# Kernel optimization log

Hardware: AMD Instinct MI355X
Metric: run time of the kernel (lower is better)

## Reference

```python
import jax, jax.numpy as jnp
import numpy as np


def setup_inputs() -> dict:
    key = jax.random.key(0)
    k1, k2, k3, k4 = jax.random.split(key, 4)
    B, C_ORIG, H, W = 64, 448, 56, 56
    C = 100
    P = H * W
    feats = jax.random.normal(k1, (B, C_ORIG, H, W), dtype=jnp.float32)
    mean = jax.random.normal(k2, (P, C), dtype=jnp.float32)
    icov = jax.random.normal(k3, (P, C, C), dtype=jnp.float32)
    sel_idx = jnp.sort(jax.random.randint(k4, (C,), 0, C_ORIG, dtype=jnp.int64))
    return {"feats": feats, "mean": mean, "icov": icov, "sel_idx": sel_idx,
            "image_size": 224}


def reference(feats, mean, icov, sel_idx, image_size):
    # feats: [B, C_orig, H, W]; select the PaDiM random channel subset -> [B, C, H, W]
    f = feats[:, sel_idx]
    B, C, H, W = f.shape
    # [B, H*W, C] patch-major layout as in the torch code
    f = jnp.transpose(f, (0, 2, 3, 1)).reshape(B, H * W, C)
    # Per-patch Mahalanobis distance, fully batched over all H*W patches
    # (replaces the Python loop of H*W small einsums in the original).
    diff = f - mean[None]                                   # [B, P, C]
    dist = jnp.einsum('bpi,pij,bpj->bp', diff, icov, diff)  # [B, P]
    score_map = dist.reshape(B, H, W)
    # Bilinear upsample to input resolution (align_corners=False ~ half-pixel)
    score_map = jax.image.resize(score_map, (B, image_size, image_size),
                                 method='bilinear')
    return score_map
```

## Files before the change

kernel.cpp:

```cpp
#include <hip/hip_runtime.h>
#include <hip/hip_bf16.h>

#define B_N     64
#define C_ORIG  448
#define C_SEL   100
#define CPD     112
#define HW      3136
#define IMG     224

typedef short bf16x8 __attribute__((ext_vector_type(8)));
typedef float f32x4  __attribute__((ext_vector_type(4)));

static __device__ __forceinline__ unsigned pkbf(float x, float y) {
    union { __hip_bfloat162 h; unsigned u; } c;
    c.h = __float22bfloat162_rn(float2{x, y});
    return c.u;
}
static __device__ __forceinline__ float bf2f(unsigned short h) {
    return __uint_as_float(((unsigned int)h) << 16);
}

__global__ __launch_bounds__(256) void kA_gather(const float* __restrict__ feats,
                                                 const float* __restrict__ mean,
                                                 const int* __restrict__ sel,
                                                 unsigned short* __restrict__ D)
{
    __shared__ unsigned short Dt[64 * 128];
    char* DtB = reinterpret_cast<char*>(Dt);
    const int tid = threadIdx.x;
    const int p0  = blockIdx.x * 64;
    const int b   = blockIdx.y;

    if (tid < 192) {
        int pr = tid / 3, un = 25 + tid % 3;
        *reinterpret_cast<uint2*>(DtB + pr * 256 + ((8 * un) ^ ((pr & 31) << 3)))
            = make_uint2(0u, 0u);
    }

    const int w    = tid >> 6;
    const int lane = tid & 63;
    const float* fb   = feats + (size_t)b * (C_ORIG * HW) + p0 + lane;
    const float* mrow = mean + (size_t)(p0 + lane) * C_SEL;
    const unsigned swz = (unsigned)(lane & 31) << 3;
    char* rowB = DtB + lane * 256;

    auto quad = [&](int c0) {
        int ch0 = sel[c0], ch1 = sel[c0 + 1], ch2 = sel[c0 + 2], ch3 = sel[c0 + 3];
        float4 m4 = *reinterpret_cast<const float4*>(mrow + c0);
        float v0 = fb[(size_t)ch0 * HW] - m4.x;
        float v1 = fb[(size_t)ch1 * HW] - m4.y;
        float v2 = fb[(size_t)ch2 * HW] - m4.z;
        float v3 = fb[(size_t)ch3 * HW] - m4.w;
        uint2 pk = make_uint2(pkbf(v0, v1), pkbf(v2, v3));
        *reinterpret_cast<uint2*>(rowB + (((unsigned)(2 * c0)) ^ swz)) = pk;
    };

    if (w < 3) {
#pragma unroll
        for (int q = 0; q < 6; ++q) quad(w * 24 + q * 4);
    } else {
#pragma unroll
        for (int q = 0; q < 7; ++q) quad(72 + q * 4);
    }
    __syncthreads();

    unsigned short* Dp = D + ((size_t)p0 * B_N + b) * CPD;
#pragma unroll
    for (int q = 0; q < 4; ++q) {
        int unit = tid + q * 256;
        if (unit < 896) {
            int pr = unit / 14;
            int s  = unit % 14;
            unsigned off = ((unsigned)(16 * s)) ^ ((((unsigned)pr & 31u) << 3) & 0xF0u);
            uint4 v = *reinterpret_cast<const uint4*>(DtB + pr * 256 + off);
            uint4 r = (pr & 1) ? make_uint4(v.z, v.w, v.x, v.y) : v;
            *reinterpret_cast<uint4*>(reinterpret_cast<char*>(Dp)
                + (size_t)pr * (B_N * CPD * 2) + s * 16) = r;
        }
    }
}

__global__ __launch_bounds__(256, 5) void kB_maha(const float* __restrict__ icov,
                                                  const unsigned short* __restrict__ D,
                                                  float* __restrict__ dist)
{
    __shared__ unsigned short Mb[112 * 128];
    char* MbB = reinterpret_cast<char*>(Mb);
    const int tid  = threadIdx.x;
    const int p    = blockIdx.x;
    const int w    = tid >> 6;
    const int lane = tid & 63;
    const int lrow = lane & 15;
    const int g    = lane >> 4;
    const int bcol = w * 16 + lrow;
    const unsigned short* Drow = D + ((size_t)p * B_N + bcol) * CPD;

    bf16x8 bfr[4];
#pragma unroll
    for (int ks = 0; ks < 4; ++ks)
        bfr[ks] = *reinterpret_cast<const bf16x8*>(Drow + ks * 32 + g * 8);
    ushort4 dvec[7];
#pragma unroll
    for (int it = 0; it < 7; ++it)
        dvec[it] = *reinterpret_cast<const ushort4*>(Drow + it * 16 + g * 4);

#pragma unroll
    for (int q = 0; q < 3; ++q) {
        int z = tid + q * 256;
        if (z < 700) {
            int i = z / 7, un = 25 + z % 7;
            *reinterpret_cast<uint2*>(MbB + i * 256 + ((8 * un) ^ ((i & 7) << 4)))
                = make_uint2(0u, 0u);
        }
    }
#pragma unroll
    for (int q = 0; q < 2; ++q) {
        int z = tid + q * 256;
        if (z < 384) {
            int i = 100 + (z >> 5), un = z & 31;
            *reinterpret_cast<uint2*>(MbB + i * 256 + ((8 * un) ^ ((i & 7) << 4)))
                = make_uint2(0u, 0u);
        }
    }
    const float4* src = reinterpret_cast<const float4*>(icov + (size_t)p * (C_SEL * C_SEL));
#pragma unroll
    for (int q = 0; q < 10; ++q) {
        int idx4 = tid + q * 256;
        if (idx4 < 2500) {
            float4 v = src[idx4];
            int i = idx4 / 25, un = idx4 % 25;
            uint2 pk = make_uint2(pkbf(v.x, v.y), pkbf(v.z, v.w));
            *reinterpret_cast<uint2*>(MbB + i * 256 + ((8 * un) ^ ((i & 7) << 4))) = pk;
        }
    }
    __syncthreads();

    f32x4 acc[7];
#pragma unroll
    for (int it = 0; it < 7; ++it) acc[it] = (f32x4){0.f, 0.f, 0.f, 0.f};

#pragma unroll
    for (int ks = 0; ks < 4; ++ks) {
#pragma unroll
        for (int it = 0; it < 7; ++it) {
            int i = it * 16 + lrow;
            bf16x8 afrag = *reinterpret_cast<const bf16x8*>(
                MbB + i * 256 + ((ks * 64 + g * 16) ^ ((i & 7) << 4)));
            acc[it] = __builtin_amdgcn_mfma_f32_16x16x32_bf16(afrag, bfr[ks], acc[it], 0, 0, 0);
        }
    }

    float partial = 0.f;
#pragma unroll
    for (int it = 0; it < 7; ++it) {
#pragma unroll
        for (int r = 0; r < 4; ++r) {
            int i = it * 16 + g * 4 + r;
            if (i < C_SEL) {
                unsigned short dh = (r == 0) ? dvec[it].x : (r == 1) ? dvec[it].y
                                   : (r == 2) ? dvec[it].z : dvec[it].w;
                partial += acc[it][r] * bf2f(dh);
            }
        }
    }
    partial += __shfl_xor(partial, 16);
    partial += __shfl_xor(partial, 32);
    if (g == 0) dist[(size_t)bcol * HW + p] = partial;
}

__global__ __launch_bounds__(256) void kC_resize(const float* __restrict__ dist,
                                                 float* __restrict__ out)
{
    int gid = blockIdx.x * 256 + threadIdx.x;
    int m = gid % 56;
    int t = gid / 56;
    int y = t % IMG;
    int b = t / IMG;

    float sy = y * 0.25f - 0.375f;
    float fy0 = floorf(sy);
    float fy = sy - fy0;
    int y0 = max((int)fy0, 0);
    int y1 = min((int)fy0 + 1, 55);
    int xm1 = max(m - 1, 0);
    int xp1 = min(m + 1, 55);

    const float* db = dist + (size_t)b * HW;
    const float* d0 = db + y0 * 56;
    const float* d1 = db + y1 * 56;
    float a0 = d0[xm1], b0 = d0[m], c0 = d0[xp1];
    float a1 = d1[xm1], b1 = d1[m], c1 = d1[xp1];

    float A  = a0 + fy * (a1 - a0);
    float Bv = b0 + fy * (b1 - b0);
    float Cv = c0 + fy * (c1 - c0);

    float4 o;
    o.x = A  + 0.625f * (Bv - A);
    o.y = A  + 0.875f * (Bv - A);
    o.z = Bv + 0.125f * (Cv - Bv);
    o.w = Bv + 0.375f * (Cv - Bv);
    *reinterpret_cast<float4*>(out + ((size_t)b * IMG + y) * IMG + 4 * m) = o;
}

extern "C" void kernel_launch(void* const* d_in, const int* in_sizes, int n_in,
                              void* d_out, int out_size, void* d_ws, size_t ws_size,
                              hipStream_t stream)
{
    const float* feats = (const float*)d_in[0];
    const float* mean  = (const float*)d_in[1];
    const float* icov  = (const float*)d_in[2];
    const int*   sel   = (const int*)d_in[3];
    float* out = (float*)d_out;

    unsigned short* Dws = (unsigned short*)d_ws;
    float* distws = (float*)((char*)d_ws + (size_t)HW * B_N * CPD * 2);

    dim3 gA(49, B_N);
    kA_gather<<<gA, 256, 0, stream>>>(feats, mean, sel, Dws);
    kB_maha<<<HW, 256, 0, stream>>>(icov, Dws, distws);
    kC_resize<<<3136, 256, 0, stream>>>(distws, out);
}
```

Baseline: 78.42 us.

## Transpose mean, store dist patch-major, and tile resize through LDS

A new pre-kernel transposes mean to channel-major so the gather kernel reads it coalesced across lanes, where it previously used strided float4 row loads. The Mahalanobis kernel now writes dist as [P][B] so its per-patch stores are contiguous, and the dvec loads move after the LDS fill. The resize kernel now runs one block per output row, staging two source rows for all batches in padded shared memory before interpolating. The cost is an extra launch and workspace buffer, and the resize grid shrinks to 224 blocks, which lowers parallelism.

```diff
diff --git a/kernel.cpp b/kernel.cpp
--- a/kernel.cpp
+++ b/kernel.cpp
@@ -20,8 +20,39 @@
     return __uint_as_float(((unsigned int)h) << 16);
 }
 
+__global__ __launch_bounds__(256) void kA0_meanT(const float* __restrict__ mean,
+                                                 float* __restrict__ meanT)
+{
+    __shared__ float mt[64 * 100];
+    const int tid = threadIdx.x;
+    const int p0  = blockIdx.x * 64;
+    const float4* src = reinterpret_cast<const float4*>(mean + (size_t)p0 * C_SEL);
+#pragma unroll
+    for (int q = 0; q < 7; ++q) {
+        int idx4 = tid + q * 256;
+        if (idx4 < 1600) {
+            float4 v = src[idx4];
+            *reinterpret_cast<float4*>(&mt[idx4 * 4]) = v;
+        }
+    }
+    __syncthreads();
+#pragma unroll
+    for (int q = 0; q < 7; ++q) {
+        int u = tid + q * 256;
+        if (u < 1600) {
+            int c = u >> 4, s = u & 15;
+            float4 v;
+            v.x = mt[(s * 4 + 0) * 100 + c];
+            v.y = mt[(s * 4 + 1) * 100 + c];
+            v.z = mt[(s * 4 + 2) * 100 + c];
+            v.w = mt[(s * 4 + 3) * 100 + c];
+            *reinterpret_cast<float4*>(meanT + (size_t)c * HW + p0 + s * 4) = v;
+        }
+    }
+}
+
 __global__ __launch_bounds__(256) void kA_gather(const float* __restrict__ feats,
-                                                 const float* __restrict__ mean,
+                                                 const float* __restrict__ meanT,
                                                  const int* __restrict__ sel,
                                                  unsigned short* __restrict__ D)
 {
@@ -39,18 +70,17 @@
 
     const int w    = tid >> 6;
     const int lane = tid & 63;
-    const float* fb   = feats + (size_t)b * (C_ORIG * HW) + p0 + lane;
-    const float* mrow = mean + (size_t)(p0 + lane) * C_SEL;
+    const float* fb = feats + (size_t)b * (C_ORIG * HW) + p0 + lane;
+    const float* mb = meanT + p0 + lane;
     const unsigned swz = (unsigned)(lane & 31) << 3;
     char* rowB = DtB + lane * 256;
 
     auto quad = [&](int c0) {
         int ch0 = sel[c0], ch1 = sel[c0 + 1], ch2 = sel[c0 + 2], ch3 = sel[c0 + 3];
-        float4 m4 = *reinterpret_cast<const float4*>(mrow + c0);
-        float v0 = fb[(size_t)ch0 * HW] - m4.x;
-        float v1 = fb[(size_t)ch1 * HW] - m4.y;
-        float v2 = fb[(size_t)ch2 * HW] - m4.z;
-        float v3 = fb[(size_t)ch3 * HW] - m4.w;
+        float v0 = fb[(size_t)ch0 * HW] - mb[(size_t)(c0 + 0) * HW];
+        float v1 = fb[(size_t)ch1 * HW] - mb[(size_t)(c0 + 1) * HW];
+        float v2 = fb[(size_t)ch2 * HW] - mb[(size_t)(c0 + 2) * HW];
+        float v3 = fb[(size_t)ch3 * HW] - mb[(size_t)(c0 + 3) * HW];
         uint2 pk = make_uint2(pkbf(v0, v1), pkbf(v2, v3));
         *reinterpret_cast<uint2*>(rowB + (((unsigned)(2 * c0)) ^ swz)) = pk;
     };
@@ -99,10 +129,6 @@
 #pragma unroll
     for (int ks = 0; ks < 4; ++ks)
         bfr[ks] = *reinterpret_cast<const bf16x8*>(Drow + ks * 32 + g * 8);
-    ushort4 dvec[7];
-#pragma unroll
-    for (int it = 0; it < 7; ++it)
-        dvec[it] = *reinterpret_cast<const ushort4*>(Drow + it * 16 + g * 4);
 
 #pragma unroll
     for (int q = 0; q < 3; ++q) {
@@ -135,6 +161,11 @@
     }
     __syncthreads();
 
+    ushort4 dvec[7];
+#pragma unroll
+    for (int it = 0; it < 7; ++it)
+        dvec[it] = *reinterpret_cast<const ushort4*>(Drow + it * 16 + g * 4);
+
     f32x4 acc[7];
 #pragma unroll
     for (int it = 0; it < 7; ++it) acc[it] = (f32x4){0.f, 0.f, 0.f, 0.f};
@@ -165,42 +196,64 @@
     }
     partial += __shfl_xor(partial, 16);
     partial += __shfl_xor(partial, 32);
-    if (g == 0) dist[(size_t)bcol * HW + p] = partial;
+    if (g == 0) dist[p * B_N + bcol] = partial;
 }
 
 __global__ __launch_bounds__(256) void kC_resize(const float* __restrict__ dist,
                                                  float* __restrict__ out)
 {
-    int gid = blockIdx.x * 256 + threadIdx.x;
-    int m = gid % 56;
-    int t = gid / 56;
-    int y = t % IMG;
-    int b = t / IMG;
+    __shared__ float L[2 * 56 * 66];
+    const int tid = threadIdx.x;
+    const int y   = blockIdx.x;
 
     float sy = y * 0.25f - 0.375f;
     float fy0 = floorf(sy);
     float fy = sy - fy0;
     int y0 = max((int)fy0, 0);
     int y1 = min((int)fy0 + 1, 55);
-    int xm1 = max(m - 1, 0);
-    int xp1 = min(m + 1, 55);
-
-    const float* db = dist + (size_t)b * HW;
-    const float* d0 = db + y0 * 56;
-    const float* d1 = db + y1 * 56;
-    float a0 = d0[xm1], b0 = d0[m], c0 = d0[xp1];
-    float a1 = d1[xm1], b1 = d1[m], c1 = d1[xp1];
-
-    float A  = a0 + fy * (a1 - a0);
-    float Bv = b0 + fy * (b1 - b0);
-    float Cv = c0 + fy * (c1 - c0);
-
-    float4 o;
-    o.x = A  + 0.625f * (Bv - A);
-    o.y = A  + 0.875f * (Bv - A);
-    o.z = Bv + 0.125f * (Cv - Bv);
-    o.w = Bv + 0.375f * (Cv - Bv);
-    *reinterpret_cast<float4*>(out + ((size_t)b * IMG + y) * IMG + 4 * m) = o;
+    int rsrc[2] = {y0, y1};
+
+#pragma unroll
+    for (int r = 0; r < 2; ++r) {
+        const float4* s4 = reinterpret_cast<const float4*>(dist + (size_t)rsrc[r] * 56 * B_N);
+#pragma unroll
+        for (int j = 0; j < 4; ++j) {
+            int idx = tid + j * 256;
+            if (idx < 896) {
+                float4 v = s4[idx];
+                int m  = idx >> 4;
+                int b4 = (idx & 15) * 4;
+                float* d = &L[r * 56 * 66 + m * 66 + b4];
+                d[0] = v.x; d[1] = v.y; d[2] = v.z; d[3] = v.w;
+            }
+        }
+    }
+    __syncthreads();
+
+#pragma unroll
+    for (int j = 0; j < 14; ++j) {
+        int unit = tid + j * 256;
+        int b = unit / 56;
+        int m = unit % 56;
+        int xm1 = max(m - 1, 0);
+        int xp1 = min(m + 1, 55);
+
+        const float* L0 = &L[0 * 56 * 66];
+        const float* L1 = &L[1 * 56 * 66];
+        float a0 = L0[xm1 * 66 + b], b0 = L0[m * 66 + b], c0 = L0[xp1 * 66 + b];
+        float a1 = L1[xm1 * 66 + b], b1 = L1[m * 66 + b], c1 = L1[xp1 * 66 + b];
+
+        float A  = a0 + fy * (a1 - a0);
+        float Bv = b0 + fy * (b1 - b0);
+        float Cv = c0 + fy * (c1 - c0);
+
+        float4 o;
+        o.x = A  + 0.625f * (Bv - A);
+        o.y = A  + 0.875f * (Bv - A);
+        o.z = Bv + 0.125f * (Cv - Bv);
+        o.w = Bv + 0.375f * (Cv - Bv);
+        *reinterpret_cast<float4*>(out + ((size_t)b * IMG + y) * IMG + 4 * m) = o;
+    }
 }
 
 extern "C" void kernel_launch(void* const* d_in, const int* in_sizes, int n_in,
@@ -213,11 +266,16 @@
     const int*   sel   = (const int*)d_in[3];
     float* out = (float*)d_out;
 
-    unsigned short* Dws = (unsigned short*)d_ws;
-    float* distws = (float*)((char*)d_ws + (size_t)HW * B_N * CPD * 2);
-
+    char* ws = (char*)d_ws;
+    unsigned short* Dws = (unsigned short*)ws;
+    size_t off = (size_t)HW * B_N * CPD * 2;
+    float* distws = (float*)(ws + off);
+    off += (size_t)HW * B_N * 4;
+    float* meanT = (float*)(ws + off);
+
+    kA0_meanT<<<49, 256, 0, stream>>>(mean, meanT);
     dim3 gA(49, B_N);
-    kA_gather<<<gA, 256, 0, stream>>>(feats, mean, sel, Dws);
+    kA_gather<<<gA, 256, 0, stream>>>(feats, meanT, sel, Dws);
     kB_maha<<<HW, 256, 0, stream>>>(icov, Dws, distws);
-    kC_resize<<<3136, 256, 0, stream>>>(distws, out);
-}
+    kC_resize<<<IMG, 256, 0, stream>>>(distws, out);
+}
```

After: 76.88 us. 2.0% less time.
